# Optimization experiments

Hardware: AMD Instinct MI355X
Metric: run time of the kernel (lower is better)

The kernel has to match this reference:

```python
import jax, jax.numpy as jnp
import numpy as np

HIDDEN = 1024
HEADS = 16
N, T1, T2 = 2, 2048, 2048


def setup_inputs() -> dict:
    key = jax.random.key(0)
    k1, k2, k3, k4 = jax.random.split(key, 4)
    q = jax.random.normal(k1, (N, T1, HIDDEN), dtype=jnp.float32)
    encoder_k = jax.random.normal(k2, (N, T2, HIDDEN), dtype=jnp.float32)
    encoder_v = jax.random.normal(k3, (N, T2, HIDDEN), dtype=jnp.float32)
    encoder_attention_mask = jnp.zeros((N, 1, T2, T2), dtype=jnp.float32)
    wo_w = jax.random.normal(k4, (HIDDEN, HIDDEN), dtype=jnp.float32) * (1.0 / np.sqrt(HIDDEN))
    wo_b = jnp.zeros((HIDDEN,), dtype=jnp.float32)
    return {"q": q, "encoder_k": encoder_k, "encoder_v": encoder_v,
            "encoder_attention_mask": encoder_attention_mask,
            "wo_w": wo_w, "wo_b": wo_b}


def _split_heads(x):
    # [N, T, E] -> [N, h, T, d]
    n, t, e = x.shape
    return x.reshape(n, t, HEADS, e // HEADS).transpose(0, 2, 1, 3)


def reference(q, encoder_k, encoder_v, encoder_attention_mask, wo_w, wo_b):
    qh = _split_heads(q)            # [N,h,T1,d]
    kh = _split_heads(encoder_k)    # [N,h,T2,d]
    vh = _split_heads(encoder_v)    # [N,h,T2,d]
    # NOTE: original applies no 1/sqrt(d) scaling
    scores = jnp.einsum('bhqd,bhkd->bhqk', qh, kh) + encoder_attention_mask
    weights = jax.nn.softmax(scores, axis=-1)
    ctx = jnp.einsum('bhqk,bhkd->bhqd', weights, vh)   # [N,h,T1,d]
    ctx = ctx.transpose(0, 2, 1, 3).reshape(q.shape[0], q.shape[1], -1)  # [N,T1,E]
    # wo: Linear (torch: x @ W.T + b) followed by ReLU
    return jax.nn.relu(ctx @ wo_w.T + wo_b)
```

## Files before the change

### kernel.cpp

```cpp
#include <hip/hip_runtime.h>
#include <hip/hip_bf16.h>


typedef short short8 __attribute__((ext_vector_type(8)));
typedef short short4v __attribute__((ext_vector_type(4)));
typedef float floatx4 __attribute__((ext_vector_type(4)));

#define HIDDEN 1024
#define HEADS 16
#define NB 2
#define T1 2048
#define T2 2048

#define LOG2E 1.44269504f
#define SHIFT 28.8539004f
#define VS 68

__device__ __forceinline__ unsigned short f2bf(float f) {
    unsigned u = __float_as_uint(f);
    return (unsigned short)((u + 0x7fffu + ((u >> 16) & 1u)) >> 16);
}

__device__ __forceinline__ short f2bf_native(float f) {
    __hip_bfloat16 h = __float2bfloat16(f);
    return __builtin_bit_cast(short, h);
}

__global__ void zero_kernel(unsigned* f) {
    if (threadIdx.x == 0) *f = 0u;
}

__global__ void prep_kernel(const float4* __restrict__ ek, const float4* __restrict__ ev,
                            const float4* __restrict__ ww, const float4* __restrict__ mask,
                            ushort4* __restrict__ dst, unsigned* __restrict__ flag) {
    const int NK = NB * T2 * HIDDEN / 4;
    const int NW = HIDDEN * HIDDEN / 4;
    if (blockIdx.y == 0) {
        int i = blockIdx.x * blockDim.x + threadIdx.x;
        int stride = gridDim.x * blockDim.x;
        const int n = 2 * NK + NW;
        for (; i < n; i += stride) {
            float4 v = (i < NK) ? ek[i] : (i < 2 * NK) ? ev[i - NK] : ww[i - 2 * NK];
            ushort4 o;
            o.x = f2bf(v.x); o.y = f2bf(v.y); o.z = f2bf(v.z); o.w = f2bf(v.w);
            dst[i] = o;
        }
    } else {
        const int NM = NB * T2 * T2 / 4;
        int i = blockIdx.x * blockDim.x + threadIdx.x;
        int stride = gridDim.x * blockDim.x;
        float mx = 0.f;
        for (; i < NM; i += stride) {
            float4 v = mask[i];
            mx = fmaxf(mx, fmaxf(fmaxf(fabsf(v.x), fabsf(v.y)), fmaxf(fabsf(v.z), fabsf(v.w))));
        }
        for (int d = 32; d; d >>= 1) mx = fmaxf(mx, __shfl_xor(mx, d));
        if ((threadIdx.x & 63) == 0 && mx > 0.f) atomicMax(flag, __float_as_uint(mx));
    }
}

__device__ __forceinline__ void stage_v(short* __restrict__ buf, const short* __restrict__ Vb,
                                        int b, int h, int kc, int tid) {
#pragma unroll
    for (int it = 0; it < 2; ++it) {
        int i = tid + (it << 8);
        int key = i & 63, dg = i >> 6;
        short8 s = *(const short8*)&Vb[(((b * T2) + kc + key) << 10) + (h << 6) + (dg << 3)];
#pragma unroll
        for (int j = 0; j < 8; ++j) buf[(dg * 8 + j) * VS + key] = s[j];
    }
}

__global__ __launch_bounds__(256) void attn_kernel(
        const float* __restrict__ q,
        const short* __restrict__ Kb,
        const short* __restrict__ Vb,
        const float* __restrict__ mask,
        const unsigned* __restrict__ flagp,
        short* __restrict__ ctx)
{
    __shared__ short lV[2][64 * VS];

    const int tid = threadIdx.x;
    const int wave = tid >> 6;
    const int lane = tid & 63;
    const int quad = lane >> 4;
    const int l16 = lane & 15;

    const int b = blockIdx.z;
    const int h = blockIdx.y;
    const int q0 = blockIdx.x * 128;

    const bool use_mask = (*flagp != 0u);

    short8 qf[2][2];
#pragma unroll
    for (int rb = 0; rb < 2; ++rb) {
#pragma unroll
        for (int ks = 0; ks < 2; ++ks) {
            const float* qp = q + (((b * T1) + q0 + wave * 32 + rb * 16 + l16) << 10)
                                + (h << 6) + ks * 32 + quad * 8;
            float4 v0 = *(const float4*)qp;
            float4 v1 = *(const float4*)(qp + 4);
            short8 s;
            s[0] = (short)f2bf(v0.x * LOG2E); s[1] = (short)f2bf(v0.y * LOG2E);
            s[2] = (short)f2bf(v0.z * LOG2E); s[3] = (short)f2bf(v0.w * LOG2E);
            s[4] = (short)f2bf(v1.x * LOG2E); s[5] = (short)f2bf(v1.y * LOG2E);
            s[6] = (short)f2bf(v1.z * LOG2E); s[7] = (short)f2bf(v1.w * LOG2E);
            qf[rb][ks] = s;
        }
    }

    floatx4 o_acc[2][4];
#pragma unroll
    for (int rb = 0; rb < 2; ++rb)
#pragma unroll
        for (int cb = 0; cb < 4; ++cb) o_acc[rb][cb] = (floatx4){0.f, 0.f, 0.f, 0.f};
    float l_st[2] = {0.f, 0.f};

    stage_v(lV[0], Vb, b, h, 0, tid);
    __syncthreads();

    for (int ic = 0; ic < T2 / 64; ++ic) {
        const int kc = ic << 6;
        const short* cur = lV[ic & 1];
        if (ic + 1 < T2 / 64) stage_v(lV[(ic + 1) & 1], Vb, b, h, kc + 64, tid);

        short8 kfrag[4][2];
#pragma unroll
        for (int kb = 0; kb < 4; ++kb)
#pragma unroll
            for (int ks = 0; ks < 2; ++ks)
                kfrag[kb][ks] = *(const short8*)
                    &Kb[(((b * T2) + kc + kb * 16 + l16) << 10) + (h << 6) + ks * 32 + quad * 8];

        short4v vfrag[4][4];
#pragma unroll
        for (int kb = 0; kb < 4; ++kb)
#pragma unroll
            for (int cb = 0; cb < 4; ++cb)
                vfrag[kb][cb] = *(const short4v*)&cur[(cb * 16 + l16) * VS + kb * 16 + quad * 4];

#pragma unroll
        for (int rb = 0; rb < 2; ++rb) {
            floatx4 st[4];
#pragma unroll
            for (int kb = 0; kb < 4; ++kb) {
                floatx4 a = (floatx4){0.f, 0.f, 0.f, 0.f};
                a = __builtin_amdgcn_mfma_f32_16x16x32_bf16(kfrag[kb][0], qf[rb][0], a, 0, 0, 0);
                a = __builtin_amdgcn_mfma_f32_16x16x32_bf16(kfrag[kb][1], qf[rb][1], a, 0, 0, 0);
                st[kb] = a;
            }
            if (use_mask) {
                int qrow = q0 + wave * 32 + rb * 16 + l16;
#pragma unroll
                for (int kb = 0; kb < 4; ++kb)
#pragma unroll
                    for (int r = 0; r < 4; ++r) {
                        int key = kc + kb * 16 + quad * 4 + r;
                        st[kb][r] += mask[(b * T2 + qrow) * T2 + key] * LOG2E;
                    }
            }
            float rs = 0.f;
            short4v pf[4];
#pragma unroll
            for (int kb = 0; kb < 4; ++kb) {
                float p0 = exp2f(st[kb][0] - SHIFT);
                float p1 = exp2f(st[kb][1] - SHIFT);
                float p2 = exp2f(st[kb][2] - SHIFT);
                float p3 = exp2f(st[kb][3] - SHIFT);
                rs += (p0 + p1) + (p2 + p3);
                pf[kb][0] = f2bf_native(p0);
                pf[kb][1] = f2bf_native(p1);
                pf[kb][2] = f2bf_native(p2);
                pf[kb][3] = f2bf_native(p3);
            }
            rs += __shfl_xor(rs, 16);
            rs += __shfl_xor(rs, 32);
            l_st[rb] += rs;

#pragma unroll
            for (int kb = 0; kb < 4; ++kb)
#pragma unroll
                for (int cb = 0; cb < 4; ++cb)
                    o_acc[rb][cb] = __builtin_amdgcn_mfma_f32_16x16x16bf16_1k(
                        vfrag[kb][cb], pf[kb], o_acc[rb][cb], 0, 0, 0);
        }
        __syncthreads();
    }

#pragma unroll
    for (int rb = 0; rb < 2; ++rb) {
        float rinv = 1.0f / l_st[rb];
        int qrow = q0 + wave * 32 + rb * 16 + l16;
#pragma unroll
        for (int cb = 0; cb < 4; ++cb) {
            short4v o;
#pragma unroll
            for (int r = 0; r < 4; ++r) o[r] = (short)f2bf(o_acc[rb][cb][r] * rinv);
            *(short4v*)&ctx[((b * T1 + qrow) << 10) + (h << 6) + cb * 16 + quad * 4] = o;
        }
    }
}

__global__ __launch_bounds__(512) void proj_kernel(
        const short* __restrict__ Cb,
        const short* __restrict__ Wb,
        const float* __restrict__ bias,
        float* __restrict__ out)
{
    __shared__ short lA[2][128 * 72];
    __shared__ short lB[2][128 * 72];

    const int tid = threadIdx.x;
    const int wave = tid >> 6;
    const int lane = tid & 63;
    const int quad = lane >> 4;
    const int l16 = lane & 15;
    const int wm = wave >> 2, wn = wave & 3;
    const int bm = blockIdx.x, bn = blockIdx.y;

    floatx4 acc[4][2];
#pragma unroll
    for (int i = 0; i < 4; ++i)
#pragma unroll
        for (int j = 0; j < 2; ++j) acc[i][j] = (floatx4){0.f, 0.f, 0.f, 0.f};

    short8 ra[2], rbw[2];
#pragma unroll
    for (int it = 0; it < 2; ++it) {
        int i = tid + it * 512;
        int row = i >> 3, c = i & 7;
        ra[it]  = *(const short8*)&Cb[((bm * 128 + row) << 10) + c * 8];
        rbw[it] = *(const short8*)&Wb[((bn * 128 + row) << 10) + c * 8];
    }
#pragma unroll
    for (int it = 0; it < 2; ++it) {
        int i = tid + it * 512;
        int row = i >> 3, c = i & 7;
        *(short8*)&lA[0][row * 72 + c * 8] = ra[it];
        *(short8*)&lB[0][row * 72 + c * 8] = rbw[it];
    }
    __syncthreads();

    int cur = 0;
    for (int kt = 0; kt < 1024; kt += 64) {
        const bool has_next = (kt + 64 < 1024);
        if (has_next) {
#pragma unroll
            for (int it = 0; it < 2; ++it) {
                int i = tid + it * 512;
                int row = i >> 3, c = i & 7;
                ra[it]  = *(const short8*)&Cb[((bm * 128 + row) << 10) + kt + 64 + c * 8];
                rbw[it] = *(const short8*)&Wb[((bn * 128 + row) << 10) + kt + 64 + c * 8];
            }
        }

#pragma unroll
        for (int ks = 0; ks < 2; ++ks) {
            short8 af[4], bf[2];
#pragma unroll
            for (int i = 0; i < 4; ++i)
                af[i] = *(const short8*)&lA[cur][(wm * 64 + i * 16 + l16) * 72 + ks * 32 + quad * 8];
#pragma unroll
            for (int j = 0; j < 2; ++j)
                bf[j] = *(const short8*)&lB[cur][(wn * 32 + j * 16 + l16) * 72 + ks * 32 + quad * 8];
#pragma unroll
            for (int i = 0; i < 4; ++i)
#pragma unroll
                for (int j = 0; j < 2; ++j)
                    acc[i][j] = __builtin_amdgcn_mfma_f32_16x16x32_bf16(af[i], bf[j], acc[i][j], 0, 0, 0);
        }

        if (has_next) {
#pragma unroll
            for (int it = 0; it < 2; ++it) {
                int i = tid + it * 512;
                int row = i >> 3, c = i & 7;
                *(short8*)&lA[cur ^ 1][row * 72 + c * 8] = ra[it];
                *(short8*)&lB[cur ^ 1][row * 72 + c * 8] = rbw[it];
            }
        }
        __syncthreads();
        cur ^= 1;
    }

    float bv[2];
#pragma unroll
    for (int j = 0; j < 2; ++j) bv[j] = bias[bn * 128 + wn * 32 + j * 16 + l16];

#pragma unroll
    for (int i = 0; i < 4; ++i)
#pragma unroll
        for (int j = 0; j < 2; ++j)
#pragma unroll
            for (int r = 0; r < 4; ++r) {
                int row = bm * 128 + wm * 64 + i * 16 + quad * 4 + r;
                int col = bn * 128 + wn * 32 + j * 16 + l16;
                float v = acc[i][j][r] + bv[j];
                out[(row << 10) + col] = fmaxf(v, 0.f);
            }
}

extern "C" void kernel_launch(void* const* d_in, const int* in_sizes, int n_in,
                              void* d_out, int out_size, void* d_ws, size_t ws_size,
                              hipStream_t stream) {
    const float* q    = (const float*)d_in[0];
    const float* ek   = (const float*)d_in[1];
    const float* ev   = (const float*)d_in[2];
    const float* mask = (const float*)d_in[3];
    const float* wo_w = (const float*)d_in[4];
    const float* wo_b = (const float*)d_in[5];
    float* out = (float*)d_out;

    char* ws = (char*)d_ws;
    unsigned* flag = (unsigned*)ws;
    short* Kb = (short*)(ws + 4096);
    short* Vb = Kb + (NB * T2 * HIDDEN);
    short* Wb = Vb + (NB * T2 * HIDDEN);
    short* Cb = Wb + (HIDDEN * HIDDEN);

    zero_kernel<<<1, 64, 0, stream>>>(flag);
    prep_kernel<<<dim3(512, 2), 256, 0, stream>>>(
        (const float4*)ek, (const float4*)ev, (const float4*)wo_w, (const float4*)mask,
        (ushort4*)Kb, flag);
    attn_kernel<<<dim3(T1 / 128, HEADS, NB), 256, 0, stream>>>(q, Kb, Vb, mask, flag, Cb);
    proj_kernel<<<dim3(32, 8), 512, 0, stream>>>(Cb, Wb, wo_b, out);
}
```

Measured before the change: 244.1 us.

## Software-pipeline K and V global loads one chunk ahead in attention loop

Prefetches the next chunk's K fragments and V tile into registers at the start of each iteration. The V tile is written into the alternate LDS buffer only after the MFMA work is done. Global load latency should then overlap the score/softmax/PV compute instead of stalling before it. Launch bounds now request 2 blocks per CU, which limits registers even though the prefetch buffers raise register pressure, so spills are possible.

```diff
diff --git a/kernel.cpp b/kernel.cpp
--- a/kernel.cpp
+++ b/kernel.cpp
@@ -71,7 +71,7 @@
     }
 }
 
-__global__ __launch_bounds__(256) void attn_kernel(
+__global__ __launch_bounds__(256, 2) void attn_kernel(
         const float* __restrict__ q,
         const short* __restrict__ Kb,
         const short* __restrict__ Vb,
@@ -119,20 +119,36 @@
     float l_st[2] = {0.f, 0.f};
 
     stage_v(lV[0], Vb, b, h, 0, tid);
+    short8 kfrag[4][2];
+#pragma unroll
+    for (int kb = 0; kb < 4; ++kb)
+#pragma unroll
+        for (int ks = 0; ks < 2; ++ks)
+            kfrag[kb][ks] = *(const short8*)
+                &Kb[(((b * T2) + kb * 16 + l16) << 10) + (h << 6) + ks * 32 + quad * 8];
     __syncthreads();
 
     for (int ic = 0; ic < T2 / 64; ++ic) {
         const int kc = ic << 6;
         const short* cur = lV[ic & 1];
-        if (ic + 1 < T2 / 64) stage_v(lV[(ic + 1) & 1], Vb, b, h, kc + 64, tid);
-
-        short8 kfrag[4][2];
+        const bool has_next = (ic + 1 < T2 / 64);
+        const int kcn = has_next ? kc + 64 : kc;
+
+        short8 vreg[2];
+#pragma unroll
+        for (int it = 0; it < 2; ++it) {
+            int i = tid + (it << 8);
+            int key = i & 63, dg = i >> 6;
+            vreg[it] = *(const short8*)&Vb[(((b * T2) + kcn + key) << 10) + (h << 6) + (dg << 3)];
+        }
+
+        short8 knext[4][2];
 #pragma unroll
         for (int kb = 0; kb < 4; ++kb)
 #pragma unroll
             for (int ks = 0; ks < 2; ++ks)
-                kfrag[kb][ks] = *(const short8*)
-                    &Kb[(((b * T2) + kc + kb * 16 + l16) << 10) + (h << 6) + ks * 32 + quad * 8];
+                knext[kb][ks] = *(const short8*)
+                    &Kb[(((b * T2) + kcn + kb * 16 + l16) << 10) + (h << 6) + ks * 32 + quad * 8];
 
         short4v vfrag[4][4];
 #pragma unroll
@@ -186,6 +202,24 @@
                     o_acc[rb][cb] = __builtin_amdgcn_mfma_f32_16x16x16bf16_1k(
                         vfrag[kb][cb], pf[kb], o_acc[rb][cb], 0, 0, 0);
         }
+
+        if (has_next) {
+            short* nbuf = lV[(ic + 1) & 1];
+#pragma unroll
+            for (int it = 0; it < 2; ++it) {
+                int i = tid + (it << 8);
+                int key = i & 63, dg = i >> 6;
+#pragma unroll
+                for (int j = 0; j < 8; ++j) nbuf[(dg * 8 + j) * VS + key] = vreg[it][j];
+            }
+        }
+
+#pragma unroll
+        for (int kb = 0; kb < 4; ++kb)
+#pragma unroll
+            for (int ks = 0; ks < 2; ++ks)
+                kfrag[kb][ks] = knext[kb][ks];
+
         __syncthreads();
     }
 
```

Measured after the change: 227.8 us. 6.7% less time.
